# Kernel tuning notes

Measured on AMD Instinct MI355X. Metric: run time of the kernel, lower is better.

The kernel has to match this reference:

```python
import jax, jax.numpy as jnp
import numpy as np

B, S, H, D = 2, 2048, 16, 128


def setup_inputs() -> dict:
    key = jax.random.key(0)
    kq, kk, kv = jax.random.split(key, 3)
    return {
        "query": jax.random.normal(kq, (B, S, H, D), dtype=jnp.float32),
        "key": jax.random.normal(kk, (B, S, H, D), dtype=jnp.float32),
        "value": jax.random.normal(kv, (B, S, H, D), dtype=jnp.float32),
    }


def reference(query, key, value):
    # Single-device semantics of HybridAttention: the Ulysses all-to-alls are
    # resharding collectives (identity at world_size=1); the ring flash-attn
    # computes standard causal scaled-dot-product attention over the full seq.
    d = query.shape[-1]
    scale = 1.0 / jnp.sqrt(jnp.asarray(d, dtype=query.dtype))
    # [b, h, q, k]
    scores = jnp.einsum("bqhd,bkhd->bhqk", query, key) * scale
    s = query.shape[1]
    causal_mask = jnp.tril(jnp.ones((s, s), dtype=bool))  # [q, k]
    scores = jnp.where(causal_mask[None, None], scores, jnp.finfo(scores.dtype).min)
    probs = jax.nn.softmax(scores, axis=-1)
    out = jnp.einsum("bhqk,bkhd->bqhd", probs, value)
    return out
```

## Files before the change

### kernel.cpp

```cpp
#include <hip/hip_runtime.h>
#include <hip/hip_bf16.h>

constexpr int Bc = 2, Sc = 2048, Hc = 16, Dc = 128;
constexpr int RS = Hc * Dc;
constexpr float SCALE2 = 0.08838834764831845f * 1.4426950408889634f;

constexpr int QBLK = 128;
constexpr int KVBLK = 32;
constexpr int NW = 8;
constexpr int NQB = Sc / QBLK;
constexpr int KPAD = Dc + 8;
constexpr int VPAD = KVBLK;
constexpr int PPAD = KVBLK + 8;

typedef __attribute__((ext_vector_type(8))) short bf16x8;
typedef __attribute__((ext_vector_type(4))) float f32x4;

__device__ __forceinline__ unsigned short f2b(float f) {
  return __builtin_bit_cast(unsigned short, __float2bfloat16(f));
}

__global__ __launch_bounds__(512, 4)
void fa_fwd(const float* __restrict__ Q, const float* __restrict__ K,
            const float* __restrict__ V, float* __restrict__ O) {
  __shared__ unsigned short Klds[2][KVBLK][KPAD];
  __shared__ unsigned short Vt[2][Dc][VPAD];
  __shared__ unsigned short Plds[NW][16][PPAD];

  const int tid = threadIdx.x;
  const int wid = tid >> 6;
  const int lane = tid & 63;
  const int lq = lane & 15;
  const int g = lane >> 4;

  const int n = blockIdx.x;
  const int bh = n & 31;
  const int a = (n >> 5) & 7;
  const int qblk = (n < 256) ? a : 15 - a;
  const int b = bh >> 4;
  const int h = bh & 15;

  const int q0 = qblk * QBLK;
  const int qw = q0 + wid * 16;

  const size_t base = (size_t)b * Sc * RS + (size_t)h * Dc;
  const float* Qp = Q + base;
  const float* Kp = K + base;
  const float* Vp = V + base;
  float* Op = O + base;

  bf16x8 qf[4];
  {
    const float* qrow = Qp + (size_t)(qw + lq) * RS + 8 * g;
    #pragma unroll
    for (int c = 0; c < 4; ++c) {
      float4 f0 = *(const float4*)(qrow + 32 * c);
      float4 f1 = *(const float4*)(qrow + 32 * c + 4);
      bf16x8 v;
      v[0] = (short)f2b(f0.x * SCALE2); v[1] = (short)f2b(f0.y * SCALE2);
      v[2] = (short)f2b(f0.z * SCALE2); v[3] = (short)f2b(f0.w * SCALE2);
      v[4] = (short)f2b(f1.x * SCALE2); v[5] = (short)f2b(f1.y * SCALE2);
      v[6] = (short)f2b(f1.z * SCALE2); v[7] = (short)f2b(f1.w * SCALE2);
      qf[c] = v;
    }
  }

  f32x4 acc[8];
  #pragma unroll
  for (int dc = 0; dc < 8; ++dc) acc[dc] = f32x4{0.f, 0.f, 0.f, 0.f};
  float l_r[4] = {0.f, 0.f, 0.f, 0.f};

  const int nkv = (q0 + QBLK) / KVBLK;

  const int krow = tid >> 3;
  const int kseg = tid & 7;
  const int vt_ = tid & 255;
  const int vrow = vt_ & 31;
  const int vseg = vt_ >> 5;

  float4 sreg[4];
  auto issue = [&](int kv0) {
    if (wid < 4) {
      const float4* ks = (const float4*)(Kp + (size_t)(kv0 + krow) * RS + kseg * 16);
      sreg[0] = ks[0]; sreg[1] = ks[1]; sreg[2] = ks[2]; sreg[3] = ks[3];
    } else {
      const float4* vs = (const float4*)(Vp + (size_t)(kv0 + vrow) * RS + vseg * 16);
      sreg[0] = vs[0]; sreg[1] = vs[1]; sreg[2] = vs[2]; sreg[3] = vs[3];
    }
  };
  auto commit = [&](int buf) {
    if (wid < 4) {
      const float* kf = (const float*)sreg;
      bf16x8 w0, w1;
      #pragma unroll
      for (int e = 0; e < 8; ++e) { w0[e] = (short)f2b(kf[e]); w1[e] = (short)f2b(kf[8 + e]); }
      *(bf16x8*)&Klds[buf][krow][kseg * 16] = w0;
      *(bf16x8*)&Klds[buf][krow][kseg * 16 + 8] = w1;
    } else {
      const float* vf = (const float*)sreg;
      #pragma unroll
      for (int e = 0; e < 16; ++e) Vt[buf][vseg * 16 + e][vrow] = f2b(vf[e]);
    }
  };

  issue(0);
  commit(0);
  __syncthreads();

  for (int kb = 0; kb < nkv; ++kb) {
    const int kv0 = kb * KVBLK;
    const int p = kb & 1;
    const bool pf = (kb + 1 < nkv);

    if (pf) issue(kv0 + KVBLK);

    const bool dead = (kv0 > qw + 15);
    if (!dead) {
      f32x4 s0 = {0.f, 0.f, 0.f, 0.f}, s1 = {0.f, 0.f, 0.f, 0.f};
      #pragma unroll
      for (int c = 0; c < 4; ++c) {
        bf16x8 k0 = *(const bf16x8*)&Klds[p][lq][32 * c + 8 * g];
        bf16x8 k1 = *(const bf16x8*)&Klds[p][16 + lq][32 * c + 8 * g];
        s0 = __builtin_amdgcn_mfma_f32_16x16x32_bf16(qf[c], k0, s0, 0, 0, 0);
        s1 = __builtin_amdgcn_mfma_f32_16x16x32_bf16(qf[c], k1, s1, 0, 0, 0);
      }

      bf16x8 vfr[8];
      #pragma unroll
      for (int dc = 0; dc < 8; ++dc)
        vfr[dc] = *(const bf16x8*)&Vt[p][16 * dc + lq][8 * g];

      const bool nomask = (kv0 + KVBLK - 1) <= qw;
      #pragma unroll
      for (int r = 0; r < 4; ++r) {
        float sa = s0[r], sb = s1[r];
        if (!nomask) {
          const int qrow = qw + 4 * g + r;
          sa = (kv0 + lq      > qrow) ? -1e30f : sa;
          sb = (kv0 + 16 + lq > qrow) ? -1e30f : sb;
        }
        const float p0 = __builtin_amdgcn_exp2f(sa);
        const float p1 = __builtin_amdgcn_exp2f(sb);
        Plds[wid][4 * g + r][lq] = f2b(p0);
        Plds[wid][4 * g + r][16 + lq] = f2b(p1);
        l_r[r] += p0 + p1;
      }

      const bf16x8 pa = *(const bf16x8*)&Plds[wid][lq][8 * g];
      #pragma unroll
      for (int dc = 0; dc < 8; ++dc)
        acc[dc] = __builtin_amdgcn_mfma_f32_16x16x32_bf16(pa, vfr[dc], acc[dc], 0, 0, 0);
    }

    if (pf) commit(p ^ 1);
    __syncthreads();
  }

  float inv[4];
  #pragma unroll
  for (int r = 0; r < 4; ++r) {
    float l = l_r[r];
    #pragma unroll
    for (int o = 8; o >= 1; o >>= 1) l += __shfl_xor(l, o);
    inv[r] = 1.0f / l;
  }
  float* orow = Op + (size_t)(qw + 4 * g) * RS + lq;
  #pragma unroll
  for (int dc = 0; dc < 8; ++dc) {
    #pragma unroll
    for (int r = 0; r < 4; ++r)
      orow[(size_t)r * RS + 16 * dc] = acc[dc][r] * inv[r];
  }
}

extern "C" void kernel_launch(void* const* d_in, const int* in_sizes, int n_in,
                              void* d_out, int out_size, void* d_ws, size_t ws_size,
                              hipStream_t stream) {
  const float* Q = (const float*)d_in[0];
  const float* K = (const float*)d_in[1];
  const float* V = (const float*)d_in[2];
  float* O = (float*)d_out;
  fa_fwd<<<dim3(NQB * Bc * Hc), dim3(512), 0, stream>>>(Q, K, V, O);
}
```

Measured before the change: 84.70 us.

## Swizzle K/V shared-memory layout and spread staging loads across all warps

Replaces the padded K and transposed-V LDS arrays with XOR-swizzled unpadded layouts to avoid bank conflicts. The global-to-LDS staging now has every thread load both K and V, instead of warps 0-3 loading K and 4-7 loading V. V is written to LDS as packed bf16 pairs (32-bit stores) rather than 16 scalar 16-bit stores. V fragment reads move inside the PV MFMA loop, which lowers register pressure but may expose LDS latency.

```diff
diff --git a/kernel.cpp b/kernel.cpp
--- a/kernel.cpp
+++ b/kernel.cpp
@@ -9,22 +9,24 @@
 constexpr int KVBLK = 32;
 constexpr int NW = 8;
 constexpr int NQB = Sc / QBLK;
-constexpr int KPAD = Dc + 8;
-constexpr int VPAD = KVBLK;
-constexpr int PPAD = KVBLK + 8;
+constexpr int PPAD = 40;
 
 typedef __attribute__((ext_vector_type(8))) short bf16x8;
 typedef __attribute__((ext_vector_type(4))) float f32x4;
+typedef __attribute__((ext_vector_type(4))) unsigned int u32x4;
 
 __device__ __forceinline__ unsigned short f2b(float f) {
   return __builtin_bit_cast(unsigned short, __float2bfloat16(f));
+}
+__device__ __forceinline__ unsigned int pk2(float lo, float hi) {
+  return (unsigned int)f2b(lo) | ((unsigned int)f2b(hi) << 16);
 }
 
 __global__ __launch_bounds__(512, 4)
 void fa_fwd(const float* __restrict__ Q, const float* __restrict__ K,
             const float* __restrict__ V, float* __restrict__ O) {
-  __shared__ unsigned short Klds[2][KVBLK][KPAD];
-  __shared__ unsigned short Vt[2][Dc][VPAD];
+  __shared__ unsigned short Kl[2][KVBLK * Dc];
+  __shared__ unsigned short Vt[2][Dc * KVBLK];
   __shared__ unsigned short Plds[NW][16][PPAD];
 
   const int tid = threadIdx.x;
@@ -72,34 +74,29 @@
 
   const int nkv = (q0 + QBLK) / KVBLK;
 
-  const int krow = tid >> 3;
-  const int kseg = tid & 7;
-  const int vt_ = tid & 255;
-  const int vrow = vt_ & 31;
-  const int vseg = vt_ >> 5;
+  const int skv = tid >> 4, sj = tid & 15;
+  const int vm = tid >> 5, vc = tid & 31;
 
-  float4 sreg[4];
+  float4 k0r, k1r, va, vb;
   auto issue = [&](int kv0) {
-    if (wid < 4) {
-      const float4* ks = (const float4*)(Kp + (size_t)(kv0 + krow) * RS + kseg * 16);
-      sreg[0] = ks[0]; sreg[1] = ks[1]; sreg[2] = ks[2]; sreg[3] = ks[3];
-    } else {
-      const float4* vs = (const float4*)(Vp + (size_t)(kv0 + vrow) * RS + vseg * 16);
-      sreg[0] = vs[0]; sreg[1] = vs[1]; sreg[2] = vs[2]; sreg[3] = vs[3];
-    }
+    const float* ks = Kp + (size_t)(kv0 + skv) * RS + sj * 8;
+    k0r = ((const float4*)ks)[0];
+    k1r = ((const float4*)ks)[1];
+    const float* vs = Vp + (size_t)(kv0 + 2 * vm) * RS + vc * 4;
+    va = *(const float4*)vs;
+    vb = *(const float4*)(vs + RS);
   };
   auto commit = [&](int buf) {
-    if (wid < 4) {
-      const float* kf = (const float*)sreg;
-      bf16x8 w0, w1;
-      #pragma unroll
-      for (int e = 0; e < 8; ++e) { w0[e] = (short)f2b(kf[e]); w1[e] = (short)f2b(kf[8 + e]); }
-      *(bf16x8*)&Klds[buf][krow][kseg * 16] = w0;
-      *(bf16x8*)&Klds[buf][krow][kseg * 16 + 8] = w1;
-    } else {
-      const float* vf = (const float*)sreg;
-      #pragma unroll
-      for (int e = 0; e < 16; ++e) Vt[buf][vseg * 16 + e][vrow] = f2b(vf[e]);
+    u32x4 kw = { pk2(k0r.x, k0r.y), pk2(k0r.z, k0r.w),
+                 pk2(k1r.x, k1r.y), pk2(k1r.z, k1r.w) };
+    *(u32x4*)&Kl[buf][skv * Dc + ((sj ^ (skv & 7)) * 8)] = kw;
+    const float* ea = (const float*)&va;
+    const float* eb = (const float*)&vb;
+    #pragma unroll
+    for (int i = 0; i < 4; ++i) {
+      const int d = 4 * vc + i;
+      *(unsigned int*)&Vt[buf][d * KVBLK + (((vm >> 2) ^ (d & 3)) * 8) + 2 * (vm & 3)]
+          = pk2(ea[i], eb[i]);
     }
   };
 
@@ -119,16 +116,12 @@
       f32x4 s0 = {0.f, 0.f, 0.f, 0.f}, s1 = {0.f, 0.f, 0.f, 0.f};
       #pragma unroll
       for (int c = 0; c < 4; ++c) {
-        bf16x8 k0 = *(const bf16x8*)&Klds[p][lq][32 * c + 8 * g];
-        bf16x8 k1 = *(const bf16x8*)&Klds[p][16 + lq][32 * c + 8 * g];
-        s0 = __builtin_amdgcn_mfma_f32_16x16x32_bf16(qf[c], k0, s0, 0, 0, 0);
-        s1 = __builtin_amdgcn_mfma_f32_16x16x32_bf16(qf[c], k1, s1, 0, 0, 0);
+        const int slot = (4 * c + g) ^ (lq & 7);
+        bf16x8 kf0 = *(const bf16x8*)&Kl[p][lq * Dc + slot * 8];
+        bf16x8 kf1 = *(const bf16x8*)&Kl[p][(16 + lq) * Dc + slot * 8];
+        s0 = __builtin_amdgcn_mfma_f32_16x16x32_bf16(qf[c], kf0, s0, 0, 0, 0);
+        s1 = __builtin_amdgcn_mfma_f32_16x16x32_bf16(qf[c], kf1, s1, 0, 0, 0);
       }
-
-      bf16x8 vfr[8];
-      #pragma unroll
-      for (int dc = 0; dc < 8; ++dc)
-        vfr[dc] = *(const bf16x8*)&Vt[p][16 * dc + lq][8 * g];
 
       const bool nomask = (kv0 + KVBLK - 1) <= qw;
       #pragma unroll
@@ -145,11 +138,14 @@
         Plds[wid][4 * g + r][16 + lq] = f2b(p1);
         l_r[r] += p0 + p1;
       }
+      const bf16x8 pa = *(const bf16x8*)&Plds[wid][lq][8 * g];
 
-      const bf16x8 pa = *(const bf16x8*)&Plds[wid][lq][8 * g];
       #pragma unroll
-      for (int dc = 0; dc < 8; ++dc)
-        acc[dc] = __builtin_amdgcn_mfma_f32_16x16x32_bf16(pa, vfr[dc], acc[dc], 0, 0, 0);
+      for (int dc = 0; dc < 8; ++dc) {
+        const int d = 16 * dc + lq;
+        bf16x8 vfr = *(const bf16x8*)&Vt[p][d * KVBLK + ((g ^ (lq & 3)) * 8)];
+        acc[dc] = __builtin_amdgcn_mfma_f32_16x16x32_bf16(pa, vfr, acc[dc], 0, 0, 0);
+      }
     }
 
     if (pf) commit(p ^ 1);
```

After: 122.0 us. 44.1% more time.
